# Optimization experiments

Hardware: AMD Instinct MI355X
Metric: run time of the kernel (lower is better)

Reference implementation:

```python
import jax, jax.numpy as jnp
import numpy as np

B, T, C, H = 128, 256, 512, 512

def setup_inputs() -> dict:
    key = jax.random.key(0)
    k1, k2, k3, k4 = jax.random.split(key, 4)
    x = jax.random.normal(k1, (B, T, C), dtype=jnp.float32)
    # nn.Linear(n_embed, H_size, bias=False).weight has shape [H, C]; scaled init
    s = 1.0 / np.sqrt(C)
    Wq = jax.random.normal(k2, (H, C), dtype=jnp.float32) * s
    Wk = jax.random.normal(k3, (H, C), dtype=jnp.float32) * s
    Wv = jax.random.normal(k4, (H, C), dtype=jnp.float32) * s
    return {"x": x, "Wq": Wq, "Wk": Wk, "Wv": Wv}

def reference(x, Wq, Wk, Wv):
    # q,k,v: [B,T,H] = x @ W.T (torch Linear convention)
    q = jnp.einsum('btc,hc->bth', x, Wq)
    k = jnp.einsum('btc,hc->bth', x, Wk)
    v = jnp.einsum('btc,hc->bth', x, Wv)
    scale = k.shape[-1] ** -0.5
    score = jnp.einsum('bqh,bkh->bqk', q, k) * scale  # [B,T,T]
    # causal mask: position j attends to i only if i <= j
    i = jnp.arange(T)
    causal = i[None, :] <= i[:, None]  # [T,T] lower-triangular
    score = jnp.where(causal[None, :, :], score, -jnp.inf)
    attn = jax.nn.softmax(score, axis=-1)
    # dropout is identity in eval mode
    out = jnp.einsum('bqk,bkh->bqh', attn, v)  # [B,T,H]
    return out
```

## Files before the change

kernel.cpp:

```cpp
#include <hip/hip_runtime.h>

#define B_ 128
#define T_ 256
#define C_ 512
#define H_ 512
#define CSCALE 0.063763824f

typedef _Float16 f16x8 __attribute__((ext_vector_type(8)));
typedef _Float16 f16x4 __attribute__((ext_vector_type(4)));
typedef _Float16 f16x2 __attribute__((ext_vector_type(2)));
typedef float    f32x4 __attribute__((ext_vector_type(4)));
typedef float    f32x16 __attribute__((ext_vector_type(16)));
typedef unsigned int u32;
typedef u32 u32x4 __attribute__((ext_vector_type(4)));

__device__ __forceinline__ void gld16(const void* gsrc, void* ldst) {
  __builtin_amdgcn_global_load_lds(
      (__attribute__((address_space(1))) void*)gsrc,
      (__attribute__((address_space(3))) void*)ldst, 16, 0, 0);
}

__global__ __launch_bounds__(256) void cvt_kernel(
    const float4* __restrict__ x, const float4* __restrict__ wq,
    const float4* __restrict__ wk, const float4* __restrict__ wv,
    f16x4* __restrict__ dst) {
  const int NX = (B_ * T_ * C_) / 4;
  const int NW = (H_ * C_) / 4;
  const int total = NX + 3 * NW;
  int gid = blockIdx.x * 256 + threadIdx.x;
  int gsz = gridDim.x * 256;
  for (int i = gid; i < total; i += gsz) {
    float4 f;
    if (i < NX)            f = x[i];
    else if (i < NX + NW)  f = wq[i - NX];
    else if (i < NX + 2*NW) f = wk[i - NX - NW];
    else                   f = wv[i - NX - 2*NW];
    f16x4 u = {(_Float16)f.x, (_Float16)f.y, (_Float16)f.z, (_Float16)f.w};
    dst[i] = u;
  }
}

__global__ __launch_bounds__(256, 2) void proj_kernel(
    const _Float16* __restrict__ xh, const _Float16* __restrict__ wh,
    _Float16* __restrict__ qh, _Float16* __restrict__ kh,
    _Float16* __restrict__ vth) {
  __shared__ _Float16 L[3][2][4096];

  const int tid  = threadIdx.x;
  const int lane = tid & 63;
  const int wave = tid >> 6;
  const int lr = lane & 15, lk = lane >> 4;
  const int lane8 = lane * 8;
  const int m0 = blockIdx.x * 128;
  const int n0 = blockIdx.y * 128;
  const int z  = blockIdx.z;
  const _Float16* wz = wh + z * (H_ * C_);

  const int wm = (wave >> 1) * 64;
  const int wn = (wave & 1) * 64;
  const int ga = (wave >> 1) * 4;
  const int gb = (wave & 1) * 4;

  const _Float16* aS = xh + (size_t)(m0 + wave * 16 + lr) * C_ + lk * 8;
  const _Float16* bS = wz + (size_t)(n0 + wave * 16 + lr) * C_ + lk * 8;

  f32x4 acc[4][4];
#pragma unroll
  for (int i = 0; i < 4; ++i)
#pragma unroll
    for (int j = 0; j < 4; ++j) acc[i][j] = {0.f, 0.f, 0.f, 0.f};

#define STAGE(RB, K0) do {                                                    \
    gld16((const void*)(aS + (K0)),            (void*)&L[RB][0][wave * 512]); \
    gld16((const void*)(aS + 64 * C_ + (K0)),  (void*)&L[RB][0][(4 + wave) * 512]); \
    gld16((const void*)(bS + (K0)),            (void*)&L[RB][1][wave * 512]); \
    gld16((const void*)(bS + 64 * C_ + (K0)),  (void*)&L[RB][1][(4 + wave) * 512]); \
  } while (0)

  STAGE(0, 0);
  STAGE(1, 32);
  asm volatile("s_waitcnt vmcnt(4)" ::: "memory");
  __builtin_amdgcn_s_barrier();

#pragma unroll 1
  for (int t = 0; t < 16; ++t) {
    const int rb = t % 3;

    f16x8 af[4], bf[4];
#pragma unroll
    for (int mi = 0; mi < 4; ++mi)
      af[mi] = *(const f16x8*)&L[rb][0][(ga + mi) * 512 + lane8];
#pragma unroll
    for (int ni = 0; ni < 4; ++ni)
      bf[ni] = *(const f16x8*)&L[rb][1][(gb + ni) * 512 + lane8];

    if (t + 2 < 16) STAGE((t + 2) % 3, (t + 2) * 32);

    __builtin_amdgcn_s_setprio(1);
#pragma unroll
    for (int mi = 0; mi < 4; ++mi)
#pragma unroll
      for (int ni = 0; ni < 4; ++ni)
        acc[mi][ni] = __builtin_amdgcn_mfma_f32_16x16x32_f16(
            af[mi], bf[ni], acc[mi][ni], 0, 0, 0);
    __builtin_amdgcn_s_setprio(0);

    if (t + 2 < 16)      asm volatile("s_waitcnt vmcnt(4)" ::: "memory");
    else if (t == 14)    asm volatile("s_waitcnt vmcnt(0)" ::: "memory");
    __builtin_amdgcn_s_barrier();
  }
#undef STAGE

  if (z < 2) {
    _Float16* out = (z == 0) ? qh : kh;
#pragma unroll
    for (int mi = 0; mi < 4; ++mi) {
      int mg = m0 + wm + mi * 16 + lk * 4;
#pragma unroll
      for (int ni = 0; ni < 4; ++ni) {
        int n = n0 + wn + ni * 16 + lr;
#pragma unroll
        for (int r = 0; r < 4; ++r)
          out[(size_t)(mg + r) * H_ + n] = (_Float16)acc[mi][ni][r];
      }
    }
  } else {
#pragma unroll
    for (int mi = 0; mi < 4; ++mi) {
      int mbase = m0 + wm + mi * 16 + lk * 4;
      int bb = mbase >> 8, tt = mbase & 255;
#pragma unroll
      for (int ni = 0; ni < 4; ++ni) {
        int n = n0 + wn + ni * 16 + lr;
        f16x4 u = {(_Float16)acc[mi][ni][0], (_Float16)acc[mi][ni][1],
                   (_Float16)acc[mi][ni][2], (_Float16)acc[mi][ni][3]};
        *(f16x4*)&vth[(size_t)bb * (H_ * T_) + (size_t)n * T_ + tt] = u;
      }
    }
  }
}

__global__ __launch_bounds__(256, 2) void attn_kernel(
    const _Float16* __restrict__ qh, const _Float16* __restrict__ kh,
    const _Float16* __restrict__ vth, float* __restrict__ dout) {
  __shared__ f32x4 Ex[2][4][4][64];

  const int tid  = threadIdx.x;
  const int lane = tid & 63;
  const int wq   = tid >> 6;
  const int lq   = lane & 31;
  const int hi   = lane >> 5;
  const int flat = blockIdx.x;
  const int xcd  = flat & 7;
  const int rest = flat >> 3;
  const int qb   = 7 - (rest & 7);
  const int g    = rest >> 3;
  const int b    = xcd + (g << 3);
  const int q0   = qb * 32;
  const int nkv  = qb + 1;
  const int hbase = wq * 128;
  const int qg   = q0 + lq;

  f16x8 qf[8];
  const _Float16* qp = qh + ((size_t)b * T_ + qg) * H_ + hbase + hi * 8;
#pragma unroll
  for (int ks = 0; ks < 8; ++ks) qf[ks] = *(const f16x8*)&qp[ks * 16];

  f32x16 ot[4];
#pragma unroll
  for (int i = 0; i < 4; ++i) ot[i] = {};
  float m_ = -1e30f, l_ = 0.f;

  const _Float16* kp = kh  + ((size_t)b * T_ + lq) * H_ + hbase + hi * 8;
  const _Float16* vp = vth + ((size_t)b * H_ + hbase + lq) * T_ + hi * 8;

  f16x8 kf[8];
#pragma unroll
  for (int ks = 0; ks < 8; ++ks) kf[ks] = *(const f16x8*)&kp[ks * 16];
  {
    f32x16 s2 = {};
#pragma unroll
    for (int ks = 0; ks < 8; ++ks)
      s2 = __builtin_amdgcn_mfma_f32_32x32x16_f16(kf[ks], qf[ks], s2, 0, 0, 0);
#pragma unroll
    for (int c = 0; c < 4; ++c) {
      f32x4 w4 = {s2[c*4+0], s2[c*4+1], s2[c*4+2], s2[c*4+3]};
      Ex[0][wq][c][lane] = w4;
    }
  }

  for (int kvt = 0; kvt < nkv; ++kvt) {
    const int kv0 = kvt * 32;
    const int buf = kvt & 1;
    const bool more = (kvt + 1 < nkv);
    __syncthreads();

    f32x16 st;
#pragma unroll
    for (int c = 0; c < 4; ++c) {
      f32x4 r0 = Ex[buf][0][c][lane];
      f32x4 r1 = Ex[buf][1][c][lane];
      f32x4 r2 = Ex[buf][2][c][lane];
      f32x4 r3 = Ex[buf][3][c][lane];
      f32x4 r = (r0 + r1) + (r2 + r3);
      st[c*4+0] = r[0]; st[c*4+1] = r[1]; st[c*4+2] = r[2]; st[c*4+3] = r[3];
    }

    if (more) {
#pragma unroll
      for (int ks = 0; ks < 8; ++ks)
        kf[ks] = *(const f16x8*)&kp[(size_t)(kv0 + 32) * H_ + ks * 16];
    }

    float rm = -1e30f;
    const int kvb = kv0 + 4 * hi;
#pragma unroll
    for (int r = 0; r < 16; ++r) {
      int kvg = kvb + (r & 3) + 8 * (r >> 2);
      float v = (kvg > qg) ? -1e30f : st[r];
      st[r] = v;
      rm = fmaxf(rm, v);
    }
    rm = fmaxf(rm, __shfl_xor(rm, 32, 64));

    if (__any((int)(rm > m_ + 64.f))) {
      float mn = fmaxf(m_, rm);
      float al = __builtin_amdgcn_exp2f((m_ - mn) * CSCALE);
      m_ = mn; l_ *= al;
#pragma unroll
      for (int i = 0; i < 4; ++i)
#pragma unroll
        for (int e = 0; e < 16; ++e) ot[i][e] *= al;
    }
    float rs = 0.f;
#pragma unroll
    for (int r = 0; r < 16; ++r) {
      st[r] = __builtin_amdgcn_exp2f((st[r] - m_) * CSCALE);
      rs += st[r];
    }
    rs += __shfl_xor(rs, 32, 64);
    l_ += rs;

    f16x8 pb0, pb1;
    {
      f16x2 h0 = {(_Float16)st[0], (_Float16)st[1]};
      f16x2 h1 = {(_Float16)st[2], (_Float16)st[3]};
      f16x2 h2 = {(_Float16)st[4], (_Float16)st[5]};
      f16x2 h3 = {(_Float16)st[6], (_Float16)st[7]};
      u32 w0 = __builtin_bit_cast(u32, h0), w1 = __builtin_bit_cast(u32, h1);
      u32 w2 = __builtin_bit_cast(u32, h2), w3 = __builtin_bit_cast(u32, h3);
      u32 s0 = (u32)__shfl_xor((int)w0, 32, 64);
      u32 s1 = (u32)__shfl_xor((int)w1, 32, 64);
      u32 s2 = (u32)__shfl_xor((int)w2, 32, 64);
      u32 s3 = (u32)__shfl_xor((int)w3, 32, 64);
      u32x4 t0 = { hi ? s2 : w0, hi ? s3 : w1, hi ? w2 : s0, hi ? w3 : s1 };
      pb0 = __builtin_bit_cast(f16x8, t0);
    }
    {
      f16x2 h0 = {(_Float16)st[8],  (_Float16)st[9]};
      f16x2 h1 = {(_Float16)st[10], (_Float16)st[11]};
      f16x2 h2 = {(_Float16)st[12], (_Float16)st[13]};
      f16x2 h3 = {(_Float16)st[14], (_Float16)st[15]};
      u32 w0 = __builtin_bit_cast(u32, h0), w1 = __builtin_bit_cast(u32, h1);
      u32 w2 = __builtin_bit_cast(u32, h2), w3 = __builtin_bit_cast(u32, h3);
      u32 s0 = (u32)__shfl_xor((int)w0, 32, 64);
      u32 s1 = (u32)__shfl_xor((int)w1, 32, 64);
      u32 s2 = (u32)__shfl_xor((int)w2, 32, 64);
      u32 s3 = (u32)__shfl_xor((int)w3, 32, 64);
      u32x4 t1 = { hi ? s2 : w0, hi ? s3 : w1, hi ? w2 : s0, hi ? w3 : s1 };
      pb1 = __builtin_bit_cast(f16x8, t1);
    }

    __builtin_amdgcn_s_setprio(1);
#pragma unroll
    for (int ht = 0; ht < 4; ++ht) {
      f16x8 va0 = *(const f16x8*)&vp[(size_t)(ht * 32) * T_ + kv0];
      f16x8 va1 = *(const f16x8*)&vp[(size_t)(ht * 32) * T_ + kv0 + 16];
      ot[ht] = __builtin_amdgcn_mfma_f32_32x32x16_f16(va0, pb0, ot[ht], 0, 0, 0);
      ot[ht] = __builtin_amdgcn_mfma_f32_32x32x16_f16(va1, pb1, ot[ht], 0, 0, 0);
    }
    __builtin_amdgcn_s_setprio(0);

    if (more) {
      f32x16 s2v = {};
      __builtin_amdgcn_s_setprio(1);
#pragma unroll
      for (int ks = 0; ks < 8; ++ks)
        s2v = __builtin_amdgcn_mfma_f32_32x32x16_f16(kf[ks], qf[ks], s2v, 0, 0, 0);
      __builtin_amdgcn_s_setprio(0);
#pragma unroll
      for (int c = 0; c < 4; ++c) {
        f32x4 w4 = {s2v[c*4+0], s2v[c*4+1], s2v[c*4+2], s2v[c*4+3]};
        Ex[buf ^ 1][wq][c][lane] = w4;
      }
    }
  }

  float li = 1.0f / l_;
  float* op = dout + ((size_t)b * T_ + qg) * H_ + hbase + 4 * hi;
#pragma unroll
  for (int ht = 0; ht < 4; ++ht)
#pragma unroll
    for (int rq = 0; rq < 4; ++rq) {
      f32x4 v4 = {ot[ht][rq*4+0] * li, ot[ht][rq*4+1] * li,
                  ot[ht][rq*4+2] * li, ot[ht][rq*4+3] * li};
      *(f32x4*)&op[ht * 32 + rq * 8] = v4;
    }
}

extern "C" void kernel_launch(void* const* d_in, const int* in_sizes, int n_in,
                              void* d_out, int out_size, void* d_ws, size_t ws_size,
                              hipStream_t stream) {
  const size_t NXE = (size_t)B_ * T_ * C_;
  const size_t NWE = (size_t)3 * H_ * C_;
  const size_t NQE = (size_t)B_ * T_ * H_;
  const size_t need = (NXE + NWE + 3 * NQE) * sizeof(_Float16);
  if (ws_size < need) return;

  const float* x  = (const float*)d_in[0];
  const float* wq = (const float*)d_in[1];
  const float* wk = (const float*)d_in[2];
  const float* wv = (const float*)d_in[3];

  _Float16* xh  = (_Float16*)d_ws;
  _Float16* wh  = xh + NXE;
  _Float16* qh  = wh + NWE;
  _Float16* kh  = qh + NQE;
  _Float16* vth = kh + NQE;

  cvt_kernel<<<2048, 256, 0, stream>>>((const float4*)x, (const float4*)wq,
                                       (const float4*)wk, (const float4*)wv,
                                       (f16x4*)xh);
  proj_kernel<<<dim3(256, 4, 3), dim3(256), 0, stream>>>(xh, wh, qh, kh, vth);
  attn_kernel<<<1024, 256, 0, stream>>>(qh, kh, vth, (float*)d_out);
}
```

Before: 202.0 us.

## Fuse Q/K/V projections into one block sharing the X tile, drop pipelining

The projection kernel now computes all three Q, K and V outputs in each block. It uses a 128x64 tile per weight, so each loaded X tile is reused across three weights, and the grid drops from 256x4x3 to 256x8. This is meant to cut redundant global reads of X, which were previously fetched once per projection. In exchange it removes the triple-buffered async load pipeline and its fine-grained waitcnt scheduling, replacing it with a simple synchronous load-sync-compute loop. It also raises launch bounds to 3 blocks per CU, which limits registers while 24 accumulators per wave must stay live.

```diff
diff --git a/kernel.cpp b/kernel.cpp
--- a/kernel.cpp
+++ b/kernel.cpp
@@ -40,11 +40,12 @@
   }
 }
 
-__global__ __launch_bounds__(256, 2) void proj_kernel(
+__global__ __launch_bounds__(256, 3) void proj_kernel(
     const _Float16* __restrict__ xh, const _Float16* __restrict__ wh,
     _Float16* __restrict__ qh, _Float16* __restrict__ kh,
     _Float16* __restrict__ vth) {
-  __shared__ _Float16 L[3][2][4096];
+  __shared__ _Float16 As[8][512];
+  __shared__ _Float16 Bs[3][4][512];
 
   const int tid  = threadIdx.x;
   const int lane = tid & 63;
@@ -52,90 +53,82 @@
   const int lr = lane & 15, lk = lane >> 4;
   const int lane8 = lane * 8;
   const int m0 = blockIdx.x * 128;
-  const int n0 = blockIdx.y * 128;
-  const int z  = blockIdx.z;
-  const _Float16* wz = wh + z * (H_ * C_);
+  const int n0 = blockIdx.y * 64;
 
   const int wm = (wave >> 1) * 64;
-  const int wn = (wave & 1) * 64;
+  const int wn = (wave & 1) * 32;
   const int ga = (wave >> 1) * 4;
-  const int gb = (wave & 1) * 4;
-
-  const _Float16* aS = xh + (size_t)(m0 + wave * 16 + lr) * C_ + lk * 8;
-  const _Float16* bS = wz + (size_t)(n0 + wave * 16 + lr) * C_ + lk * 8;
-
-  f32x4 acc[4][4];
-#pragma unroll
-  for (int i = 0; i < 4; ++i)
-#pragma unroll
-    for (int j = 0; j < 4; ++j) acc[i][j] = {0.f, 0.f, 0.f, 0.f};
-
-#define STAGE(RB, K0) do {                                                    \
-    gld16((const void*)(aS + (K0)),            (void*)&L[RB][0][wave * 512]); \
-    gld16((const void*)(aS + 64 * C_ + (K0)),  (void*)&L[RB][0][(4 + wave) * 512]); \
-    gld16((const void*)(bS + (K0)),            (void*)&L[RB][1][wave * 512]); \
-    gld16((const void*)(bS + 64 * C_ + (K0)),  (void*)&L[RB][1][(4 + wave) * 512]); \
-  } while (0)
-
-  STAGE(0, 0);
-  STAGE(1, 32);
-  asm volatile("s_waitcnt vmcnt(4)" ::: "memory");
-  __builtin_amdgcn_s_barrier();
+  const int gb = (wave & 1) * 2;
+
+  const _Float16* aS  = xh + (size_t)(m0 + wave * 16 + lr) * C_ + lk * 8;
+  const _Float16* bS0 = wh + (size_t)(n0 + wave * 16 + lr) * C_ + lk * 8;
+  const _Float16* bS1 = bS0 + (size_t)H_ * C_;
+  const _Float16* bS2 = bS1 + (size_t)H_ * C_;
+
+  f32x4 acc[3][4][2];
+#pragma unroll
+  for (int z = 0; z < 3; ++z)
+#pragma unroll
+    for (int i = 0; i < 4; ++i)
+#pragma unroll
+      for (int j = 0; j < 2; ++j) acc[z][i][j] = {0.f, 0.f, 0.f, 0.f};
 
 #pragma unroll 1
-  for (int t = 0; t < 16; ++t) {
-    const int rb = t % 3;
-
-    f16x8 af[4], bf[4];
+  for (int k0 = 0; k0 < C_; k0 += 32) {
+    __syncthreads();
+    gld16((const void*)(aS + k0),           (void*)&As[wave][0]);
+    gld16((const void*)(aS + 64 * C_ + k0), (void*)&As[4 + wave][0]);
+    gld16((const void*)(bS0 + k0),          (void*)&Bs[0][wave][0]);
+    gld16((const void*)(bS1 + k0),          (void*)&Bs[1][wave][0]);
+    gld16((const void*)(bS2 + k0),          (void*)&Bs[2][wave][0]);
+    __syncthreads();
+
+    f16x8 af[4];
 #pragma unroll
     for (int mi = 0; mi < 4; ++mi)
-      af[mi] = *(const f16x8*)&L[rb][0][(ga + mi) * 512 + lane8];
-#pragma unroll
-    for (int ni = 0; ni < 4; ++ni)
-      bf[ni] = *(const f16x8*)&L[rb][1][(gb + ni) * 512 + lane8];
-
-    if (t + 2 < 16) STAGE((t + 2) % 3, (t + 2) * 32);
-
-    __builtin_amdgcn_s_setprio(1);
-#pragma unroll
-    for (int mi = 0; mi < 4; ++mi)
-#pragma unroll
-      for (int ni = 0; ni < 4; ++ni)
-        acc[mi][ni] = __builtin_amdgcn_mfma_f32_16x16x32_f16(
-            af[mi], bf[ni], acc[mi][ni], 0, 0, 0);
-    __builtin_amdgcn_s_setprio(0);
-
-    if (t + 2 < 16)      asm volatile("s_waitcnt vmcnt(4)" ::: "memory");
-    else if (t == 14)    asm volatile("s_waitcnt vmcnt(0)" ::: "memory");
-    __builtin_amdgcn_s_barrier();
-  }
-#undef STAGE
-
-  if (z < 2) {
+      af[mi] = *(const f16x8*)&As[ga + mi][lane8];
+
+#pragma unroll
+    for (int z = 0; z < 3; ++z) {
+      f16x8 bf0 = *(const f16x8*)&Bs[z][gb][lane8];
+      f16x8 bf1 = *(const f16x8*)&Bs[z][gb + 1][lane8];
+      __builtin_amdgcn_s_setprio(1);
+#pragma unroll
+      for (int mi = 0; mi < 4; ++mi) {
+        acc[z][mi][0] = __builtin_amdgcn_mfma_f32_16x16x32_f16(
+            af[mi], bf0, acc[z][mi][0], 0, 0, 0);
+        acc[z][mi][1] = __builtin_amdgcn_mfma_f32_16x16x32_f16(
+            af[mi], bf1, acc[z][mi][1], 0, 0, 0);
+      }
+      __builtin_amdgcn_s_setprio(0);
+    }
+  }
+
+#pragma unroll
+  for (int z = 0; z < 2; ++z) {
     _Float16* out = (z == 0) ? qh : kh;
 #pragma unroll
     for (int mi = 0; mi < 4; ++mi) {
       int mg = m0 + wm + mi * 16 + lk * 4;
 #pragma unroll
-      for (int ni = 0; ni < 4; ++ni) {
+      for (int ni = 0; ni < 2; ++ni) {
         int n = n0 + wn + ni * 16 + lr;
 #pragma unroll
         for (int r = 0; r < 4; ++r)
-          out[(size_t)(mg + r) * H_ + n] = (_Float16)acc[mi][ni][r];
+          out[(size_t)(mg + r) * H_ + n] = (_Float16)acc[z][mi][ni][r];
       }
     }
-  } else {
-#pragma unroll
-    for (int mi = 0; mi < 4; ++mi) {
-      int mbase = m0 + wm + mi * 16 + lk * 4;
-      int bb = mbase >> 8, tt = mbase & 255;
-#pragma unroll
-      for (int ni = 0; ni < 4; ++ni) {
-        int n = n0 + wn + ni * 16 + lr;
-        f16x4 u = {(_Float16)acc[mi][ni][0], (_Float16)acc[mi][ni][1],
-                   (_Float16)acc[mi][ni][2], (_Float16)acc[mi][ni][3]};
-        *(f16x4*)&vth[(size_t)bb * (H_ * T_) + (size_t)n * T_ + tt] = u;
-      }
+  }
+#pragma unroll
+  for (int mi = 0; mi < 4; ++mi) {
+    int mbase = m0 + wm + mi * 16 + lk * 4;
+    int bb = mbase >> 8, tt = mbase & 255;
+#pragma unroll
+    for (int ni = 0; ni < 2; ++ni) {
+      int n = n0 + wn + ni * 16 + lr;
+      f16x4 u = {(_Float16)acc[2][mi][ni][0], (_Float16)acc[2][mi][ni][1],
+                 (_Float16)acc[2][mi][ni][2], (_Float16)acc[2][mi][ni][3]};
+      *(f16x4*)&vth[(size_t)bb * (H_ * T_) + (size_t)n * T_ + tt] = u;
     }
   }
 }
@@ -331,6 +324,6 @@
   cvt_kernel<<<2048, 256, 0, stream>>>((const float4*)x, (const float4*)wq,
                                        (const float4*)wk, (const float4*)wv,
                                        (f16x4*)xh);
-  proj_kernel<<<dim3(256, 4, 3), dim3(256), 0, stream>>>(xh, wh, qh, kh, vth);
+  proj_kernel<<<dim3(256, 8), dim3(256), 0, stream>>>(xh, wh, qh, kh, vth);
   attn_kernel<<<1024, 256, 0, stream>>>(qh, kh, vth, (float*)d_out);
 }
```

Result: faster. 186.3 us (-7.8%).

## Fuse fp32-to-fp16 conversion of x into projection kernel loads

Applied to the files above, without the earlier changes.

The projection kernel now reads x directly as fp32 into LDS and converts it to fp16 in registers, so the separate pass that wrote an fp16 copy of x is gone and only the weights are still pre-converted. The pipeline moves from triple to double buffering with a full vmcnt wait each iteration, and the occupancy hint rises to 3 blocks. This removes a full read and write of x through HBM, but each projection tile (x is reread by 12 blocks) now loads twice the bytes for A, adds conversion instructions, and overlaps loads less.

```diff
diff --git a/kernel.cpp b/kernel.cpp
--- a/kernel.cpp
+++ b/kernel.cpp
@@ -20,49 +20,42 @@
       (__attribute__((address_space(3))) void*)ldst, 16, 0, 0);
 }
 
-__global__ __launch_bounds__(256) void cvt_kernel(
-    const float4* __restrict__ x, const float4* __restrict__ wq,
-    const float4* __restrict__ wk, const float4* __restrict__ wv,
-    f16x4* __restrict__ dst) {
-  const int NX = (B_ * T_ * C_) / 4;
+__global__ __launch_bounds__(256) void cvtw_kernel(
+    const float4* __restrict__ wq, const float4* __restrict__ wk,
+    const float4* __restrict__ wv, f16x4* __restrict__ dst) {
   const int NW = (H_ * C_) / 4;
-  const int total = NX + 3 * NW;
-  int gid = blockIdx.x * 256 + threadIdx.x;
-  int gsz = gridDim.x * 256;
-  for (int i = gid; i < total; i += gsz) {
-    float4 f;
-    if (i < NX)            f = x[i];
-    else if (i < NX + NW)  f = wq[i - NX];
-    else if (i < NX + 2*NW) f = wk[i - NX - NW];
-    else                   f = wv[i - NX - 2*NW];
-    f16x4 u = {(_Float16)f.x, (_Float16)f.y, (_Float16)f.z, (_Float16)f.w};
-    dst[i] = u;
-  }
-}
-
-__global__ __launch_bounds__(256, 2) void proj_kernel(
-    const _Float16* __restrict__ xh, const _Float16* __restrict__ wh,
+  int i = blockIdx.x * 256 + threadIdx.x;
+  if (i >= 3 * NW) return;
+  float4 f = (i < NW) ? wq[i] : (i < 2 * NW ? wk[i - NW] : wv[i - 2 * NW]);
+  f16x4 u = {(_Float16)f.x, (_Float16)f.y, (_Float16)f.z, (_Float16)f.w};
+  dst[i] = u;
+}
+
+__global__ __launch_bounds__(256, 3) void proj_kernel(
+    const float* __restrict__ xf, const _Float16* __restrict__ whh,
     _Float16* __restrict__ qh, _Float16* __restrict__ kh,
     _Float16* __restrict__ vth) {
-  __shared__ _Float16 L[3][2][4096];
+  __shared__ float    As[2][4096];
+  __shared__ _Float16 Bs[2][4096];
 
   const int tid  = threadIdx.x;
   const int lane = tid & 63;
   const int wave = tid >> 6;
   const int lr = lane & 15, lk = lane >> 4;
   const int lane8 = lane * 8;
+  const int lane4 = lane * 4;
   const int m0 = blockIdx.x * 128;
   const int n0 = blockIdx.y * 128;
   const int z  = blockIdx.z;
-  const _Float16* wz = wh + z * (H_ * C_);
 
   const int wm = (wave >> 1) * 64;
   const int wn = (wave & 1) * 64;
   const int ga = (wave >> 1) * 4;
   const int gb = (wave & 1) * 4;
 
-  const _Float16* aS = xh + (size_t)(m0 + wave * 16 + lr) * C_ + lk * 8;
-  const _Float16* bS = wz + (size_t)(n0 + wave * 16 + lr) * C_ + lk * 8;
+  const float* aBase = xf + (size_t)(m0 + lr) * C_ + lk * 8;
+  const _Float16* bBase =
+      whh + (size_t)z * (H_ * C_) + (size_t)(n0 + wave * 16 + lr) * C_ + lk * 8;
 
   f32x4 acc[4][4];
 #pragma unroll
@@ -70,31 +63,43 @@
 #pragma unroll
     for (int j = 0; j < 4; ++j) acc[i][j] = {0.f, 0.f, 0.f, 0.f};
 
-#define STAGE(RB, K0) do {                                                    \
-    gld16((const void*)(aS + (K0)),            (void*)&L[RB][0][wave * 512]); \
-    gld16((const void*)(aS + 64 * C_ + (K0)),  (void*)&L[RB][0][(4 + wave) * 512]); \
-    gld16((const void*)(bS + (K0)),            (void*)&L[RB][1][wave * 512]); \
-    gld16((const void*)(bS + 64 * C_ + (K0)),  (void*)&L[RB][1][(4 + wave) * 512]); \
+#define STAGE(BUF, K0) do {                                                   \
+    gld16((const void*)(aBase + (size_t)(wave)     * 16 * C_ + (K0)),         \
+          (void*)&As[BUF][(wave) * 512]);                                     \
+    gld16((const void*)(aBase + (size_t)(wave)     * 16 * C_ + (K0) + 4),     \
+          (void*)&As[BUF][(wave) * 512 + 256]);                               \
+    gld16((const void*)(aBase + (size_t)(wave + 4) * 16 * C_ + (K0)),         \
+          (void*)&As[BUF][(wave + 4) * 512]);                                 \
+    gld16((const void*)(aBase + (size_t)(wave + 4) * 16 * C_ + (K0) + 4),     \
+          (void*)&As[BUF][(wave + 4) * 512 + 256]);                           \
+    gld16((const void*)(bBase + (K0)),                                        \
+          (void*)&Bs[BUF][(wave) * 512]);                                     \
+    gld16((const void*)(bBase + 64 * C_ + (K0)),                              \
+          (void*)&Bs[BUF][(wave + 4) * 512]);                                 \
   } while (0)
 
   STAGE(0, 0);
-  STAGE(1, 32);
-  asm volatile("s_waitcnt vmcnt(4)" ::: "memory");
+  asm volatile("s_waitcnt vmcnt(0)" ::: "memory");
   __builtin_amdgcn_s_barrier();
 
-#pragma unroll 1
+#pragma unroll 2
   for (int t = 0; t < 16; ++t) {
-    const int rb = t % 3;
+    const int buf = t & 1;
+    if (t < 15) STAGE(buf ^ 1, (t + 1) * 32);
 
     f16x8 af[4], bf[4];
 #pragma unroll
-    for (int mi = 0; mi < 4; ++mi)
-      af[mi] = *(const f16x8*)&L[rb][0][(ga + mi) * 512 + lane8];
+    for (int mi = 0; mi < 4; ++mi) {
+      f32x4 lo = *(const f32x4*)&As[buf][(ga + mi) * 512 + lane4];
+      f32x4 hv = *(const f32x4*)&As[buf][(ga + mi) * 512 + 256 + lane4];
+      f16x8 a = {(_Float16)lo[0], (_Float16)lo[1], (_Float16)lo[2],
+                 (_Float16)lo[3], (_Float16)hv[0], (_Float16)hv[1],
+                 (_Float16)hv[2], (_Float16)hv[3]};
+      af[mi] = a;
+    }
 #pragma unroll
     for (int ni = 0; ni < 4; ++ni)
-      bf[ni] = *(const f16x8*)&L[rb][1][(gb + ni) * 512 + lane8];
-
-    if (t + 2 < 16) STAGE((t + 2) % 3, (t + 2) * 32);
+      bf[ni] = *(const f16x8*)&Bs[buf][(gb + ni) * 512 + lane8];
 
     __builtin_amdgcn_s_setprio(1);
 #pragma unroll
@@ -105,8 +110,7 @@
             af[mi], bf[ni], acc[mi][ni], 0, 0, 0);
     __builtin_amdgcn_s_setprio(0);
 
-    if (t + 2 < 16)      asm volatile("s_waitcnt vmcnt(4)" ::: "memory");
-    else if (t == 14)    asm volatile("s_waitcnt vmcnt(0)" ::: "memory");
+    asm volatile("s_waitcnt vmcnt(0)" ::: "memory");
     __builtin_amdgcn_s_barrier();
   }
 #undef STAGE
@@ -311,10 +315,9 @@
 extern "C" void kernel_launch(void* const* d_in, const int* in_sizes, int n_in,
                               void* d_out, int out_size, void* d_ws, size_t ws_size,
                               hipStream_t stream) {
-  const size_t NXE = (size_t)B_ * T_ * C_;
   const size_t NWE = (size_t)3 * H_ * C_;
   const size_t NQE = (size_t)B_ * T_ * H_;
-  const size_t need = (NXE + NWE + 3 * NQE) * sizeof(_Float16);
+  const size_t need = (NWE + 3 * NQE) * sizeof(_Float16);
   if (ws_size < need) return;
 
   const float* x  = (const float*)d_in[0];
@@ -322,15 +325,13 @@
   const float* wk = (const float*)d_in[2];
   const float* wv = (const float*)d_in[3];
 
-  _Float16* xh  = (_Float16*)d_ws;
-  _Float16* wh  = xh + NXE;
-  _Float16* qh  = wh + NWE;
+  _Float16* whh = (_Float16*)d_ws;
+  _Float16* qh  = whh + NWE;
   _Float16* kh  = qh + NQE;
   _Float16* vth = kh + NQE;
 
-  cvt_kernel<<<2048, 256, 0, stream>>>((const float4*)x, (const float4*)wq,
-                                       (const float4*)wk, (const float4*)wv,
-                                       (f16x4*)xh);
-  proj_kernel<<<dim3(256, 4, 3), dim3(256), 0, stream>>>(xh, wh, qh, kh, vth);
+  cvtw_kernel<<<768, 256, 0, stream>>>((const float4*)wq, (const float4*)wk,
+                                       (const float4*)wv, (f16x4*)whh);
+  proj_kernel<<<dim3(256, 4, 3), dim3(256), 0, stream>>>(x, whh, qh, kh, vth);
   attn_kernel<<<1024, 256, 0, stream>>>(qh, kh, vth, (float*)d_out);
 }
```

Measured after the change: 234.1 us. 15.9% more time.
